# Kernel optimization log

Hardware: AMD Instinct MI355X
Metric: run time of the kernel (lower is better)

Reference implementation:

```python
import jax, jax.numpy as jnp
import numpy as np

K = 10
ALPHA = 0.1


def setup_inputs() -> dict:
    key = jax.random.key(0)
    k1, k2, k3, k4 = jax.random.split(key, 4)
    N, E, D_IN, D_OUT = 100000, 3200000, 128, 64
    x = jax.random.normal(k1, (N, D_IN), dtype=jnp.float32)
    edge_index = jax.random.randint(k2, (2, E), 0, N, dtype=jnp.int64)
    W = jax.random.normal(k3, (D_IN, D_OUT), dtype=jnp.float32) / np.sqrt(D_IN)
    b = jax.random.normal(k4, (D_OUT,), dtype=jnp.float32) * 0.01
    return {"x": x, "edge_index": edge_index, "W": W, "b": b}


def reference(x, edge_index, W, b):
    N = x.shape[0]
    # gcn_norm with self-loops (PyG default for APPNP when edge_weight is None)
    loop = jnp.arange(N, dtype=edge_index.dtype)
    src = jnp.concatenate([edge_index[0], loop])  # [E+N]
    dst = jnp.concatenate([edge_index[1], loop])
    ew = jnp.ones(src.shape[0], dtype=x.dtype)
    deg = jax.ops.segment_sum(ew, dst, num_segments=N)  # in-degree incl. self-loop
    dinv = jnp.where(deg > 0, jax.lax.rsqrt(deg), 0.0)
    norm = dinv[src] * ew * dinv[dst]  # [E+N]

    # K-step personalized PageRank propagation: h = (1-alpha) * A_hat h + alpha * x
    h = x
    for _ in range(K):
        msg = h[src] * norm[:, None]  # gather + scale, [E+N, D]
        agg = jax.ops.segment_sum(msg, dst, num_segments=N)  # scatter-add
        h = (1.0 - ALPHA) * agg + ALPHA * x

    return h @ W + b
```

## Files before the change

kernel.cpp:

```cpp
#include <hip/hip_runtime.h>
#include <hip/hip_fp16.h>
#include <math.h>


#define BSH 8


__global__ void zero_i32(int* __restrict__ p, int n) {
    int i = blockIdx.x * blockDim.x + threadIdx.x;
    if (i < n) p[i] = 0;
}

__global__ void zero_dummy(__half2* __restrict__ b0, __half2* __restrict__ b1,
                           __half2* __restrict__ b2, int N) {
    int t = threadIdx.x;
    if (t >= 96) return;
    __half2* b = (t < 32) ? b0 : (t < 64) ? b1 : b2;
    b[(size_t)N * 32 + (t & 31)] = __floats2half2_rn(0.f, 0.f);
}


__global__ void __launch_bounds__(256) bucket_hist_k(const int* __restrict__ dst, int E,
                                                     int* __restrict__ bktcnt) {
    __shared__ int hist[400];
    int t = threadIdx.x;
    for (int i = t; i < 400; i += 256) hist[i] = 0;
    __syncthreads();
    int e0 = blockIdx.x * 4096 + t;
#pragma unroll
    for (int i = 0; i < 16; ++i) {
        int e = e0 + i * 256;
        if (e < E) atomicAdd(&hist[dst[e] >> BSH], 1);
    }
    __syncthreads();
    for (int b = t; b < 400; b += 256) {
        int c = hist[b];
        if (c > 0) atomicAdd(&bktcnt[b], c);
    }
}


__global__ void bucket_scan_k(const int* __restrict__ bktcnt, int nb, int E,
                              int* __restrict__ bktbase, int* __restrict__ bktcur) {
    __shared__ int s[256];
    int t = threadIdx.x;
    int C = (nb + 255) / 256;
    int b0 = t * C;
    int loc[8]; int sum = 0;
    for (int i = 0; i < C; ++i) {
        int v = (b0 + i < nb) ? bktcnt[b0 + i] : 0;
        loc[i] = sum; sum += v;
    }
    s[t] = sum; __syncthreads();
    for (int off = 1; off < 256; off <<= 1) {
        int v = (t >= off) ? s[t - off] : 0;
        __syncthreads();
        s[t] += v;
        __syncthreads();
    }
    int excl = s[t] - sum;
    for (int i = 0; i < C; ++i)
        if (b0 + i < nb) {
            int e0 = excl + loc[i];
            bktbase[b0 + i] = e0;
            bktcur[(b0 + i) * 16] = e0;
        }
    if (t == 0) bktbase[nb] = E;
}


__global__ void __launch_bounds__(256) binsort_k(const int* __restrict__ src,
                                                 const int* __restrict__ dst, int E,
                                                 int* __restrict__ bktcur,
                                                 unsigned* __restrict__ binned) {
    __shared__ int hist[400], gbase[400], lcur[400];
    int t = threadIdx.x;
    for (int i = t; i < 400; i += 256) { hist[i] = 0; lcur[i] = 0; }
    __syncthreads();

    int e0 = blockIdx.x * 4096 + t;
    unsigned rec[16]; int bk[16];
#pragma unroll
    for (int i = 0; i < 16; ++i) {
        int e = e0 + i * 256;
        if (e < E) {
            int s = src[e], d = dst[e];
            bk[i]  = d >> BSH;
            rec[i] = ((unsigned)s << BSH) | (unsigned)(d & 255);
            atomicAdd(&hist[bk[i]], 1);
        } else bk[i] = -1;
    }
    __syncthreads();
    for (int b = t; b < 400; b += 256) {
        int c = hist[b];
        if (c > 0) gbase[b] = atomicAdd(&bktcur[b * 16], c);
    }
    __syncthreads();
#pragma unroll
    for (int i = 0; i < 16; ++i) {
        if (bk[i] >= 0) {
            int loc = atomicAdd(&lcur[bk[i]], 1);
            binned[gbase[bk[i]] + loc] = rec[i];
        }
    }
}


__global__ void __launch_bounds__(256) fill2_k(const unsigned* __restrict__ binned,
                                               const int* __restrict__ bktbase,
                                               int N, int E, int NB,
                                               int* __restrict__ rowptr,
                                               float* __restrict__ dinv,
                                               int* __restrict__ col) {
    __shared__ int cnt[256], excl[256], lcur[256];
    int b = blockIdx.x, t = threadIdx.x;
    int beg = bktbase[b], end = bktbase[b + 1];
    cnt[t] = 0;
    __syncthreads();
    for (int i = beg + t; i < end; i += 256)
        atomicAdd(&cnt[binned[i] & 255u], 1);
    __syncthreads();
    int v = cnt[t];
    excl[t] = v;
    __syncthreads();
    for (int off = 1; off < 256; off <<= 1) {
        int u = (t >= off) ? excl[t - off] : 0;
        __syncthreads();
        excl[t] += u;
        __syncthreads();
    }
    int ex = excl[t] - v;
    lcur[t] = ex;
    int d = (b << BSH) + t;
    if (d < N) {
        rowptr[d] = beg + ex;
        dinv[d] = rsqrtf((float)(v + 1));
    }
    if (b == NB - 1 && t == 0) rowptr[N] = E;
    __syncthreads();
    for (int i = beg + t; i < end; i += 256) {
        unsigned r = binned[i];
        int loc = atomicAdd(&lcur[r & 255u], 1);
        col[beg + loc] = (int)(r >> BSH);
    }
}


__global__ void __launch_bounds__(256) gemm_k(const float* __restrict__ x,
                                              const float* __restrict__ W,
                                              const float* __restrict__ dinv,
                                              __half2* __restrict__ g0f,
                                              __half2* __restrict__ g0h, int N) {
    __shared__ float xs[64 * 133];
    int t = threadIdx.x;
    int n0 = blockIdx.x * 64;
    for (int f = t; f < 64 * 32; f += 256) {
        int r = f >> 5, c4 = f & 31;
        int n = n0 + r;
        float4 v = (n < N) ? ((const float4*)x)[(size_t)n * 32 + c4]
                           : make_float4(0.f, 0.f, 0.f, 0.f);
        float* dp = &xs[r * 133 + c4 * 4];
        dp[0] = v.x; dp[1] = v.y; dp[2] = v.z; dp[3] = v.w;
    }
    __syncthreads();
    int tr = t & 15, tc = t >> 4;
    int j0 = tr * 4, r0 = tc * 4;
    const float4* W4 = (const float4*)W;
    float acc[4][4] = {};
#pragma unroll 8
    for (int k = 0; k < 128; ++k) {
        float4 wv = W4[k * 16 + tr];
#pragma unroll
        for (int i = 0; i < 4; ++i) {
            float xv = xs[(r0 + i) * 133 + k];
            acc[i][0] += xv * wv.x; acc[i][1] += xv * wv.y;
            acc[i][2] += xv * wv.z; acc[i][3] += xv * wv.w;
        }
    }
    int h0 = j0 >> 1;
#pragma unroll
    for (int i = 0; i < 4; ++i) {
        int n = n0 + r0 + i;
        if (n < N) {
            float dn = dinv[n];
            __half2* gf = &g0f[(size_t)n * 32 + h0];
            gf[0] = __floats2half2_rn(acc[i][0], acc[i][1]);
            gf[1] = __floats2half2_rn(acc[i][2], acc[i][3]);
            __half2* gp = &g0h[(size_t)n * 32 + h0];
            gp[0] = __floats2half2_rn(acc[i][0] * dn, acc[i][1] * dn);
            gp[1] = __floats2half2_rn(acc[i][2] * dn, acc[i][3] * dn);
        }
    }
}


__global__ void __launch_bounds__(256) prop_k(const __half2* __restrict__ gin,
                                              const __half2* __restrict__ g0f,
                                              __half2* __restrict__ gout,
                                              float* __restrict__ outf,
                                              const int* __restrict__ rowptr,
                                              const int* __restrict__ cols,
                                              const float* __restrict__ dinv,
                                              const float* __restrict__ bias,
                                              int N, int final_step) {
    int gw = (blockIdx.x * blockDim.x + threadIdx.x) >> 6;
    int lane = threadIdx.x & 63;
    if (gw >= N) return;
    int sub = lane >> 3;
    int q   = lane & 7;

    int beg = rowptr[gw], end = rowptr[gw + 1];
    int deg = end - beg;

    const char* gb = (const char*)gin;

    float di    = dinv[gw];
    float4 giv  = *(const float4*)(gb + (size_t)gw * 128 + q * 16);
    float4 g0v4 = *(const float4*)((const char*)g0f + (size_t)gw * 128 + q * 16);

    float a[8] = {};

    for (int base = 0; base < deg; base += 32) {
        int m = deg - base; if (m > 32) m = 32;
        int l32 = lane & 31;
        int ci = cols[beg + base + (l32 < m ? l32 : 0)];
#pragma unroll
        for (int i = 0; i < 4; ++i) {
            int e = i * 8 + sub;
            int c = __shfl(ci, e, 64);
            if (base + e >= deg) c = N;
            float4 v = *(const float4*)(gb + (size_t)c * 128 + q * 16);
            const __half2* h2 = (const __half2*)&v;
#pragma unroll
            for (int u = 0; u < 4; ++u) {
                float2 f = __half22float2(h2[u]);
                a[2 * u]     += f.x;
                a[2 * u + 1] += f.y;
            }
        }
    }

#pragma unroll
    for (int off = 8; off < 64; off <<= 1) {
#pragma unroll
        for (int u = 0; u < 8; ++u) a[u] += __shfl_xor(a[u], off, 64);
    }

    if (sub == 0) {
        const __half2* gih = (const __half2*)&giv;
        const __half2* g0h2 = (const __half2*)&g0v4;
        float r[8];
#pragma unroll
        for (int u = 0; u < 4; ++u) {
            float2 gi = __half22float2(gih[u]);
            float2 g0 = __half22float2(g0h2[u]);
            r[2 * u]     = 0.9f * di * (a[2 * u]     + gi.x) + 0.1f * g0.x;
            r[2 * u + 1] = 0.9f * di * (a[2 * u + 1] + gi.y) + 0.1f * g0.y;
        }
        if (final_step) {
            float4 b0 = ((const float4*)bias)[2 * q];
            float4 b1 = ((const float4*)bias)[2 * q + 1];
            float4 o0 = make_float4(r[0] + b0.x, r[1] + b0.y, r[2] + b0.z, r[3] + b0.w);
            float4 o1 = make_float4(r[4] + b1.x, r[5] + b1.y, r[6] + b1.z, r[7] + b1.w);
            float4* op = (float4*)(outf + (size_t)gw * 64 + q * 8);
            op[0] = o0; op[1] = o1;
        } else {
            __half2 o[4];
#pragma unroll
            for (int u = 0; u < 4; ++u)
                o[u] = __floats2half2_rn(di * r[2 * u], di * r[2 * u + 1]);
            *(float4*)((char*)gout + (size_t)gw * 128 + q * 16) = *(float4*)o;
        }
    }
}


extern "C" void kernel_launch(void* const* d_in, const int* in_sizes, int n_in,
                              void* d_out, int out_size, void* d_ws, size_t ws_size,
                              hipStream_t stream) {
    const float* x  = (const float*)d_in[0];
    const int*   ei = (const int*)d_in[1];
    const float* W  = (const float*)d_in[2];
    const float* b  = (const float*)d_in[3];
    float* out = (float*)d_out;

    const int N = in_sizes[0] / 128;
    const int E = in_sizes[1] / 2;
    const int* src = ei;
    const int* dst = ei + E;
    const int NB = (N + 255) >> BSH;

    char* w = (char*)d_ws;
    size_t off = 0;
    auto alloc = [&](size_t bytes) -> void* {
        void* p = w + off;
        off += (bytes + 255) & ~(size_t)255;
        return p;
    };
    const size_t fp16buf = (size_t)(N + 1) * 32 * sizeof(__half2);
    __half2*  g0h    = (__half2*) alloc(fp16buf);
    __half2*  bufA   = (__half2*) alloc(fp16buf);
    __half2*  bufB   = (__half2*) alloc(fp16buf);
    __half2*  g0f    = (__half2*) alloc(fp16buf);
    int*      cols   = (int*)     alloc((size_t)E * 4);
    unsigned* binned = (unsigned*)alloc((size_t)E * 4);
    int*      rowptr = (int*)     alloc((size_t)(N + 1) * 4);
    int*      bktcnt = (int*)     alloc((size_t)NB * 4);
    int*      bktbase= (int*)     alloc((size_t)(NB + 1) * 4);
    int*      bktcur = (int*)     alloc((size_t)NB * 16 * 4);
    float*    dinvv  = (float*)   alloc((size_t)N * 4);

    const int nblkB = (E + 4095) / 4096;

    zero_i32<<<(NB + 255) / 256, 256, 0, stream>>>(bktcnt, NB);
    bucket_hist_k<<<nblkB, 256, 0, stream>>>(dst, E, bktcnt);
    zero_dummy<<<1, 96, 0, stream>>>(g0h, bufA, bufB, N);
    bucket_scan_k<<<1, 256, 0, stream>>>(bktcnt, NB, E, bktbase, bktcur);
    binsort_k<<<nblkB, 256, 0, stream>>>(src, dst, E, bktcur, binned);
    fill2_k<<<NB, 256, 0, stream>>>(binned, bktbase, N, E, NB, rowptr, dinvv, cols);

    gemm_k<<<(N + 63) / 64, 256, 0, stream>>>(x, W, dinvv, g0f, g0h, N);

    const int nblkP = (N * 64 + 255) / 256;
    const __half2* gin = g0h;
    __half2* pp[2] = {bufA, bufB};
    for (int k = 0; k < 10; ++k) {
        const bool fin = (k == 9);
        __half2* gout = pp[k & 1];
        prop_k<<<nblkP, 256, 0, stream>>>(gin, g0f, gout, out, rowptr, cols,
                                          dinvv, b, N, fin ? 1 : 0);
        gin = gout;
    }
}
```

Baseline: 760.1 us.

## Batch 64 neighbor gathers per chunk with pre-shifted byte offsets and fdot2 accumulation

Column indices are stored pre-multiplied by the 128-byte row stride, so the gather address is a 32-bit OR with no 64-bit multiply. The propagation loop now handles up to 64 neighbors per chunk and issues all eight 16-byte loads before accumulating, giving more loads in flight per wave. Half-to-float accumulation uses fdot2 with selector vectors instead of explicit conversions. The 32-bit offsets assume the feature buffer is under 4 GB, and the eight staged uint4 values raise register pressure.

Result: slower. 827.9 us (+8.9%).

```diff
diff --git a/kernel.cpp b/kernel.cpp
--- a/kernel.cpp
+++ b/kernel.cpp
@@ -4,6 +4,9 @@
 
 
 #define BSH 8
+
+typedef _Float16 h2_t __attribute__((ext_vector_type(2)));
+union U16 { uint4 u; h2_t h[4]; };
 
 
 __global__ void zero_i32(int* __restrict__ p, int n) {
@@ -141,7 +144,7 @@
     for (int i = beg + t; i < end; i += 256) {
         unsigned r = binned[i];
         int loc = atomicAdd(&lcur[r & 255u], 1);
-        col[beg + loc] = (int)(r >> BSH);
+        col[beg + loc] = (int)(r >> BSH) << 7;
     }
 }
 
@@ -208,36 +211,47 @@
     if (gw >= N) return;
     int sub = lane >> 3;
     int q   = lane & 7;
+    unsigned qo = (unsigned)(q << 4);
 
     int beg = rowptr[gw], end = rowptr[gw + 1];
     int deg = end - beg;
 
     const char* gb = (const char*)gin;
 
-    float di    = dinv[gw];
-    float4 giv  = *(const float4*)(gb + (size_t)gw * 128 + q * 16);
-    float4 g0v4 = *(const float4*)((const char*)g0f + (size_t)gw * 128 + q * 16);
+    float di = dinv[gw];
+    U16 gi;  gi.u  = *(const uint4*)(gb + ((size_t)gw << 7) + qo);
+    U16 g0v; g0v.u = *(const uint4*)((const char*)g0f + ((size_t)gw << 7) + qo);
+
+    const h2_t SEL_LO = {(_Float16)1.f, (_Float16)0.f};
+    const h2_t SEL_HI = {(_Float16)0.f, (_Float16)1.f};
 
     float a[8] = {};
-
-    for (int base = 0; base < deg; base += 32) {
-        int m = deg - base; if (m > 32) m = 32;
-        int l32 = lane & 31;
-        int ci = cols[beg + base + (l32 < m ? l32 : 0)];
-#pragma unroll
-        for (int i = 0; i < 4; ++i) {
-            int e = i * 8 + sub;
-            int c = __shfl(ci, e, 64);
-            if (base + e >= deg) c = N;
-            float4 v = *(const float4*)(gb + (size_t)c * 128 + q * 16);
-            const __half2* h2 = (const __half2*)&v;
-#pragma unroll
-            for (int u = 0; u < 4; ++u) {
-                float2 f = __half22float2(h2[u]);
-                a[2 * u]     += f.x;
-                a[2 * u + 1] += f.y;
+    const int DUMMY = N << 7;
+
+    for (int base = 0; base < deg; base += 64) {
+        int m = deg - base; if (m > 64) m = 64;
+        int ci = cols[beg + base + (lane < m ? lane : 0)];
+        int nch = (m + 7) >> 3;
+        U16 v[8];
+#pragma unroll
+        for (int i = 0; i < 8; ++i) {
+            if (i < nch) {
+                int e8 = i * 8 + sub;
+                int c = __shfl(ci, e8, 64);
+                if (e8 >= m) c = DUMMY;
+                v[i].u = *(const uint4*)(gb + (unsigned)(c | (int)qo));
             }
         }
+#pragma unroll
+        for (int i = 0; i < 8; ++i) {
+            if (i < nch) {
+#pragma unroll
+                for (int u = 0; u < 4; ++u) {
+                    a[2 * u]     = __builtin_amdgcn_fdot2(v[i].h[u], SEL_LO, a[2 * u],     false);
+                    a[2 * u + 1] = __builtin_amdgcn_fdot2(v[i].h[u], SEL_HI, a[2 * u + 1], false);
+                }
+            }
+        }
     }
 
 #pragma unroll
@@ -247,29 +261,28 @@
     }
 
     if (sub == 0) {
-        const __half2* gih = (const __half2*)&giv;
-        const __half2* g0h2 = (const __half2*)&g0v4;
-        float r[8];
+        float rr[8];
 #pragma unroll
         for (int u = 0; u < 4; ++u) {
-            float2 gi = __half22float2(gih[u]);
-            float2 g0 = __half22float2(g0h2[u]);
-            r[2 * u]     = 0.9f * di * (a[2 * u]     + gi.x) + 0.1f * g0.x;
-            r[2 * u + 1] = 0.9f * di * (a[2 * u + 1] + gi.y) + 0.1f * g0.y;
+            float2 gf = __half22float2(*(__half2*)&gi.h[u]);
+            float2 g0 = __half22float2(*(__half2*)&g0v.h[u]);
+            rr[2 * u]     = 0.9f * di * (a[2 * u]     + gf.x) + 0.1f * g0.x;
+            rr[2 * u + 1] = 0.9f * di * (a[2 * u + 1] + gf.y) + 0.1f * g0.y;
         }
         if (final_step) {
             float4 b0 = ((const float4*)bias)[2 * q];
             float4 b1 = ((const float4*)bias)[2 * q + 1];
-            float4 o0 = make_float4(r[0] + b0.x, r[1] + b0.y, r[2] + b0.z, r[3] + b0.w);
-            float4 o1 = make_float4(r[4] + b1.x, r[5] + b1.y, r[6] + b1.z, r[7] + b1.w);
             float4* op = (float4*)(outf + (size_t)gw * 64 + q * 8);
-            op[0] = o0; op[1] = o1;
+            op[0] = make_float4(rr[0] + b0.x, rr[1] + b0.y, rr[2] + b0.z, rr[3] + b0.w);
+            op[1] = make_float4(rr[4] + b1.x, rr[5] + b1.y, rr[6] + b1.z, rr[7] + b1.w);
         } else {
-            __half2 o[4];
-#pragma unroll
-            for (int u = 0; u < 4; ++u)
-                o[u] = __floats2half2_rn(di * r[2 * u], di * r[2 * u + 1]);
-            *(float4*)((char*)gout + (size_t)gw * 128 + q * 16) = *(float4*)o;
+            U16 o;
+#pragma unroll
+            for (int u = 0; u < 4; ++u) {
+                __half2 h = __floats2half2_rn(di * rr[2 * u], di * rr[2 * u + 1]);
+                o.h[u] = *(h2_t*)&h;
+            }
+            *(uint4*)((char*)gout + ((size_t)gw << 7) + qo) = o.u;
         }
     }
 }
```
